# Kernel tuning notes

Hardware: AMD Instinct MI355X
Metric: run time of the kernel (lower is better)

## Reference

```python
import jax, jax.numpy as jnp
import numpy as np

D_K = 128


def setup_inputs() -> dict:
    key = jax.random.key(0)
    ks = jax.random.split(key, 10)
    B, S, D, TP, TE, DK = 4, 4096, 1024, 16, 64, D_K
    sc = lambda fan_in: 1.0 / np.sqrt(fan_in)
    return {
        "x": jax.random.normal(ks[0], (B, S, D), jnp.float32),
        "time_points": jax.random.normal(ks[1], (B, TP, TE), jnp.float32),
        "Wq": jax.random.normal(ks[2], (D, DK), jnp.float32) * sc(D),
        "bq": jnp.zeros((DK,), jnp.float32),
        "Wk": jax.random.normal(ks[3], (D, DK), jnp.float32) * sc(D),
        "bk": jnp.zeros((DK,), jnp.float32),
        "Wv": jax.random.normal(ks[4], (D, DK), jnp.float32) * sc(D),
        "bv": jnp.zeros((DK,), jnp.float32),
        "Wt": jax.random.normal(ks[5], (TE, DK), jnp.float32) * sc(TE),
        "bt": jnp.zeros((DK,), jnp.float32),
    }


def reference(x, time_points, Wq, bq, Wk, bk, Wv, bv, Wt, bt):
    B, S, _ = x.shape
    Q = x @ Wq + bq              # [B,S,dk]
    K = x @ Wk + bk              # [B,S,dk]
    V = x @ Wv + bv              # [B,S,dk]
    E = time_points @ Wt + bt    # [B,TP,dk] = time_emb
    # T = repeat(E, S times along dim 1). Then T^T @ T = S * E^T E and
    # ||T||_F = sqrt(S) * ||E||_F, so we never materialize T.
    S_f = jnp.asarray(S, jnp.float32)
    EtE = jnp.einsum('btd,bte->bde', E, E)            # [B,dk,dk]
    T_norm = jnp.sqrt(S_f * jnp.sum(E * E, axis=(1, 2), keepdims=False))  # [B]
    T_scaled = (S_f * EtE) / (T_norm[:, None, None] + 1e-8)  # [B,dk,dk]
    QT = jnp.einsum('bsd,bde->bse', Q, T_scaled)      # [B,S,dk]
    scores = jnp.einsum('bse,bte->bst', QT, K)        # [B,S,S]
    scores = scores / jnp.sqrt(jnp.asarray(D_K, jnp.float32))
    attn = jax.nn.softmax(scores, axis=-1)            # [B,S,S]
    out = jnp.einsum('bst,btd->bsd', attn, V)         # [B,S,dk]
    return out, attn
```

## Files before the change

### kernel.cpp

```cpp
#include <hip/hip_runtime.h>
#include <math.h>

#define BB 4
#define SS 4096
#define DD 1024
#define TPp 16
#define TEe 64
#define DKk 128

typedef __attribute__((ext_vector_type(8))) short short8;
typedef __attribute__((ext_vector_type(4))) float floatx4;
typedef __attribute__((ext_vector_type(16))) float floatx16;

#define BSTRIDE 524288
#define WFRAG 131072

static __device__ inline short f2bf(float f) {
  union { float f; unsigned u; } v; v.f = f;
  unsigned r = v.u + 0x7fff + ((v.u >> 16) & 1);
  return (short)(r >> 16);
}
static __device__ inline float bf2f(short s) {
  union { unsigned u; float f; } v; v.u = ((unsigned)(unsigned short)s) << 16;
  return v.f;
}

__global__ __launch_bounds__(256) void temb_kernel(const float* __restrict__ tp,
                                                   const float* __restrict__ Wt,
                                                   const float* __restrict__ bt,
                                                   const float* __restrict__ bq,
                                                   float* __restrict__ Tws,
                                                   float* __restrict__ bqtws) {
  __shared__ float sE[TPp * DKk];
  __shared__ float sB[TPp];
  __shared__ float red[256];
  const int p = blockIdx.x, b = blockIdx.y;
  const int tid = threadIdx.x;
  float lsq = 0.f;
  for (int l = 0; l < 8; ++l) {
    int idx = tid + 256 * l;
    int i = idx >> 7, j = idx & 127;
    float a = bt[j];
    for (int c = 0; c < TEe; ++c)
      a += tp[((size_t)b * TPp + i) * TEe + c] * Wt[c * DKk + j];
    sE[idx] = a;
    lsq += a * a;
  }
  red[tid] = lsq;
  __syncthreads();
  for (int s2 = 128; s2 > 0; s2 >>= 1) {
    if (tid < s2) red[tid] += red[tid + s2];
    __syncthreads();
  }
  const float total = red[0];
  const float scale = (float)SS / (sqrtf((float)SS * total) + 1e-8f);
  if (tid < TPp) {
    float a = 0.f;
    for (int d2 = 0; d2 < DKk; ++d2) a += bq[d2] * sE[tid * DKk + d2];
    sB[tid] = a;
  }
  __syncthreads();
  for (int l = 0; l < 8; ++l) {
    int idx = p * 2048 + tid + 256 * l;
    int d2 = idx >> 7, e = idx & 127;
    float a = 0.f;
    #pragma unroll
    for (int t = 0; t < TPp; ++t) a += sE[t * DKk + d2] * sE[t * DKk + e];
    Tws[(size_t)b * DKk * DKk + idx] = scale * a;
  }
  if (p == 0 && tid < DKk) {
    float a = 0.f;
    #pragma unroll
    for (int t = 0; t < TPp; ++t) a += sB[t] * sE[t * DKk + tid];
    bqtws[b * DKk + tid] = scale * a;
  }
}

__global__ __launch_bounds__(128) void wqp_kernel(const float* __restrict__ Wq,
                                                  const float* __restrict__ Tws,
                                                  short* __restrict__ WqphF,
                                                  short* __restrict__ WqplF) {
  __shared__ float sW[DKk];
  const int m = blockIdx.x, b = blockIdx.y;
  const int e = threadIdx.x;
  sW[e] = Wq[(size_t)m * DKk + e];
  __syncthreads();
  const float* Tb = Tws + (size_t)b * DKk * DKk;
  float a = 0.f;
  #pragma unroll 8
  for (int d2 = 0; d2 < DKk; ++d2) a += sW[d2] * Tb[d2 * DKk + e];
  const size_t off = (size_t)b * WFRAG +
      (size_t)((e >> 5) * 64 + (m >> 4)) * 512 + (32 * ((m >> 3) & 1) + (e & 31)) * 8 +
      (m & 7);
  short hh = f2bf(a);
  WqphF[off] = hh;
  WqplF[off] = f2bf(a - bf2f(hh));
}

__global__ __launch_bounds__(256) void wcast_kernel(const float* __restrict__ Wk,
                                                    const float* __restrict__ Wv,
                                                    short* __restrict__ WkhF,
                                                    short* __restrict__ WklF,
                                                    short* __restrict__ WvhF,
                                                    short* __restrict__ WvlF) {
  const float* W = blockIdx.y ? Wv : Wk;
  short* H = blockIdx.y ? WvhF : WkhF;
  short* L = blockIdx.y ? WvlF : WklF;
  const int ks = blockIdx.x;
  const int wave = threadIdx.x >> 6, lane = threadIdx.x & 63;
  const int n = wave * 32 + (lane & 31);
  const int k0 = ks * 16 + (lane >> 5) * 8;
  short8 h, l;
  #pragma unroll
  for (int j = 0; j < 8; ++j) {
    float v = W[(size_t)(k0 + j) * DKk + n];
    short hh = f2bf(v);
    h[j] = hh;
    l[j] = f2bf(v - bf2f(hh));
  }
  const size_t off = ((size_t)wave * 64 + ks) * 512 + lane * 8;
  *(short8*)&H[off] = h;
  *(short8*)&L[off] = l;
}

__global__ __launch_bounds__(256, 2) void proj_kernel(const float* __restrict__ x,
                                                      const short* __restrict__ WqphF,
                                                      const short* __restrict__ WqplF,
                                                      const short* __restrict__ WkhF,
                                                      const short* __restrict__ WklF,
                                                      const short* __restrict__ WvhF,
                                                      const short* __restrict__ WvlF,
                                                      const float* __restrict__ bqt,
                                                      const float* __restrict__ bk,
                                                      const float* __restrict__ bv,
                                                      short* __restrict__ QTh,
                                                      short* __restrict__ QTl,
                                                      short* __restrict__ Kh,
                                                      short* __restrict__ Kl,
                                                      short* __restrict__ VT) {
  __shared__ float xs[32 * 66];
  const int tileG = blockIdx.x;
  const int b = tileG >> 7, tileL = tileG & 127;
  const int rowbase = tileG * 32;
  const int tid = threadIdx.x, wave = tid >> 6, lane = tid & 63;
  const int l31 = lane & 31, half = lane >> 5;
  const short* B0h = WqphF + (size_t)b * WFRAG + (size_t)wave * 32768;
  const short* B0l = WqplF + (size_t)b * WFRAG + (size_t)wave * 32768;
  const short* B1h = WkhF + (size_t)wave * 32768;
  const short* B1l = WklF + (size_t)wave * 32768;
  const short* B2h = WvhF + (size_t)wave * 32768;
  const short* B2l = WvlF + (size_t)wave * 32768;
  floatx16 acc0, acc1, acc2;
  #pragma unroll
  for (int r = 0; r < 16; ++r) { acc0[r] = 0.f; acc1[r] = 0.f; acc2[r] = 0.f; }
  const int sr = tid >> 3, sc = (tid & 7) * 8;
  const float* xrow = &x[(size_t)(rowbase + sr) * DD + sc];
  float4 p0 = *(const float4*)xrow;
  float4 p1 = *(const float4*)(xrow + 4);
  for (int kc = 0; kc < 16; ++kc) {
    __syncthreads();
    float* dst = &xs[sr * 66 + sc];
    dst[0] = p0.x; dst[1] = p0.y; dst[2] = p0.z; dst[3] = p0.w;
    dst[4] = p1.x; dst[5] = p1.y; dst[6] = p1.z; dst[7] = p1.w;
    if (kc < 15) {
      p0 = *(const float4*)(xrow + (kc + 1) * 64);
      p1 = *(const float4*)(xrow + (kc + 1) * 64 + 4);
    }
    __syncthreads();
    #pragma unroll
    for (int ks = 0; ks < 4; ++ks) {
      const float* ap = &xs[l31 * 66 + ks * 16 + half * 8];
      short8 aH, aL;
      #pragma unroll
      for (int j = 0; j < 8; ++j) {
        float v = ap[j];
        short hh = f2bf(v);
        aH[j] = hh;
        aL[j] = f2bf(v - bf2f(hh));
      }
      const size_t boff = (size_t)(kc * 4 + ks) * 512 + lane * 8;
      short8 bh, bl;
      bh = *(const short8*)(B0h + boff); bl = *(const short8*)(B0l + boff);
      acc0 = __builtin_amdgcn_mfma_f32_32x32x16_bf16(aL, bh, acc0, 0, 0, 0);
      acc0 = __builtin_amdgcn_mfma_f32_32x32x16_bf16(aH, bl, acc0, 0, 0, 0);
      acc0 = __builtin_amdgcn_mfma_f32_32x32x16_bf16(aH, bh, acc0, 0, 0, 0);
      bh = *(const short8*)(B1h + boff); bl = *(const short8*)(B1l + boff);
      acc1 = __builtin_amdgcn_mfma_f32_32x32x16_bf16(aL, bh, acc1, 0, 0, 0);
      acc1 = __builtin_amdgcn_mfma_f32_32x32x16_bf16(aH, bl, acc1, 0, 0, 0);
      acc1 = __builtin_amdgcn_mfma_f32_32x32x16_bf16(aH, bh, acc1, 0, 0, 0);
      bh = *(const short8*)(B2h + boff); bl = *(const short8*)(B2l + boff);
      acc2 = __builtin_amdgcn_mfma_f32_32x32x16_bf16(aL, bh, acc2, 0, 0, 0);
      acc2 = __builtin_amdgcn_mfma_f32_32x32x16_bf16(aH, bl, acc2, 0, 0, 0);
      acc2 = __builtin_amdgcn_mfma_f32_32x32x16_bf16(aH, bh, acc2, 0, 0, 0);
    }
  }
  const int f = wave * 32 + l31;
  const int fks = f >> 4, fh = (f >> 3) & 1, fj = f & 7;
  const size_t qkbase =
      (size_t)b * BSTRIDE + (size_t)tileL * 4096 + (size_t)fks * 512 + fj;
  const float biasq = bqt[b * DKk + f];
  const float biask = bk[f];
  #pragma unroll
  for (int reg = 0; reg < 16; ++reg) {
    const int t = (reg & 3) + 8 * (reg >> 2) + 4 * half;
    const size_t off = qkbase + (size_t)(fh * 32 + t) * 8;
    float v = acc0[reg] + biasq;
    short hh = f2bf(v);
    QTh[off] = hh;
    QTl[off] = f2bf(v - bf2f(hh));
    v = acc1[reg] + biask;
    hh = f2bf(v);
    Kh[off] = hh;
    Kl[off] = f2bf(v - bf2f(hh));
  }
  const float biasv = bv[f];
  const int n15 = f & 15, ntt = f >> 4;
  #pragma unroll
  for (int g = 0; g < 4; ++g) {
    short4 s4;
    s4.x = f2bf(acc2[4 * g + 0] + biasv);
    s4.y = f2bf(acc2[4 * g + 1] + biasv);
    s4.z = f2bf(acc2[4 * g + 2] + biasv);
    s4.w = f2bf(acc2[4 * g + 3] + biasv);
    const size_t off = (size_t)b * BSTRIDE + (size_t)(tileL * 8 + ntt) * 512 +
                       (size_t)(g * 16 + n15) * 8 + 4 * half;
    *(short4*)&VT[off] = s4;
  }
}

__global__ __launch_bounds__(256, 2) void score_kernel(const short* __restrict__ QTh,
                                                       const short* __restrict__ QTl,
                                                       const short* __restrict__ Kh,
                                                       const short* __restrict__ Kl,
                                                       float* __restrict__ attn,
                                                       float* __restrict__ mrow,
                                                       float* __restrict__ linv) {
  __shared__ float smM[4][32], smL[4][32];
  const int id = blockIdx.x;
  const int xcd = id & 7;
  const int b = xcd >> 1;
  const int tile = ((id >> 3) << 1) + (xcd & 1);
  const int rowbase = tile * 32;
  const int tid = threadIdx.x;
  const int wave = tid >> 6, lane = tid & 63;
  const int l31 = lane & 31, half = lane >> 5;
  const float sc = 0.088388347648318447f;
  const size_t qbase = (size_t)b * BSTRIDE + (size_t)tile * 4096 + lane * 8;
  short8 aH[8], aL[8];
  #pragma unroll
  for (int ks = 0; ks < 8; ++ks) {
    aH[ks] = *(const short8*)(QTh + qbase + ks * 512);
    aL[ks] = *(const short8*)(QTl + qbase + ks * 512);
  }
  float m_r[16], l_r[16];
  #pragma unroll
  for (int r = 0; r < 16; ++r) { m_r[r] = -INFINITY; l_r[r] = 0.f; }
  float* attnb = attn + (size_t)b * SS * SS;
  float* srowbase = attnb + (size_t)rowbase * SS + l31;
  for (int ct = wave; ct < 128; ct += 4) {
    const int colbase = ct * 32;
    const size_t kbase = (size_t)b * BSTRIDE + (size_t)ct * 4096 + lane * 8;
    floatx16 acc;
    #pragma unroll
    for (int r = 0; r < 16; ++r) acc[r] = 0.f;
    #pragma unroll
    for (int ks = 0; ks < 8; ++ks) {
      short8 bh = *(const short8*)(Kh + kbase + ks * 512);
      short8 bl = *(const short8*)(Kl + kbase + ks * 512);
      acc = __builtin_amdgcn_mfma_f32_32x32x16_bf16(aH[ks], bh, acc, 0, 0, 0);
      acc = __builtin_amdgcn_mfma_f32_32x32x16_bf16(aH[ks], bl, acc, 0, 0, 0);
      acc = __builtin_amdgcn_mfma_f32_32x32x16_bf16(aL[ks], bh, acc, 0, 0, 0);
    }
    float* srow = srowbase + colbase;
    #pragma unroll
    for (int reg = 0; reg < 16; ++reg) {
      const int row = (reg & 3) + 8 * (reg >> 2) + 4 * half;
      const float s = acc[reg] * sc;
      __builtin_nontemporal_store(s, &srow[(size_t)row * SS]);
      const float mn = fmaxf(m_r[reg], s);
      l_r[reg] = l_r[reg] * __expf(m_r[reg] - mn) + __expf(s - mn);
      m_r[reg] = mn;
    }
  }
  #pragma unroll
  for (int off = 1; off < 32; off <<= 1) {
    #pragma unroll
    for (int reg = 0; reg < 16; ++reg) {
      const float mo = __shfl_xor(m_r[reg], off, 64);
      const float lo = __shfl_xor(l_r[reg], off, 64);
      const float mn = fmaxf(m_r[reg], mo);
      l_r[reg] = l_r[reg] * __expf(m_r[reg] - mn) + lo * __expf(mo - mn);
      m_r[reg] = mn;
    }
  }
  if (l31 == 0) {
    #pragma unroll
    for (int reg = 0; reg < 16; ++reg) {
      const int row = (reg & 3) + 8 * (reg >> 2) + 4 * half;
      smM[wave][row] = m_r[reg];
      smL[wave][row] = l_r[reg];
    }
  }
  __syncthreads();
  if (tid < 32) {
    float m = smM[0][tid], l = smL[0][tid];
    #pragma unroll
    for (int w = 1; w < 4; ++w) {
      const float mo = smM[w][tid], lo = smL[w][tid];
      const float mn = fmaxf(m, mo);
      l = l * __expf(m - mn) + lo * __expf(mo - mn);
      m = mn;
    }
    mrow[b * SS + rowbase + tid] = m;
    linv[b * SS + rowbase + tid] = 1.0f / l;
  }
}

__global__ __launch_bounds__(512, 4) void pv_kernel(const short* __restrict__ VT,
                                                    float* __restrict__ attn,
                                                    const float* __restrict__ mrow,
                                                    const float* __restrict__ linv,
                                                    float* __restrict__ outp) {
  __shared__ float sAcc[3][2][16][128];
  const int id = blockIdx.x;
  const int xcd = id & 7;
  const int b = xcd >> 1;
  const int tile = ((id >> 3) << 1) + (xcd & 1);
  const int rowbase = tile * 32;
  const int tid = threadIdx.x, wave = tid >> 6, lane = tid & 63;
  const int wg = wave & 1, th = wave >> 1;
  const int l15 = lane & 15, quad = lane >> 4;
  const int row = rowbase + wg * 16 + l15;
  const float m_i = mrow[b * SS + row];
  const float li = linv[b * SS + row];
  float* arow = attn + (size_t)b * SS * SS + (size_t)row * SS + quad * 8;
  const short* vtb = VT + (size_t)b * BSTRIDE + lane * 8;
  floatx4 acc[8];
  #pragma unroll
  for (int nt = 0; nt < 8; ++nt)
    #pragma unroll
    for (int r = 0; r < 4; ++r) acc[nt][r] = 0.f;
  for (int ct = th; ct < 128; ct += 4) {
    const int t0 = ct * 32;
    floatx4 s0 = __builtin_nontemporal_load((const floatx4*)(arow + t0));
    floatx4 s1 = __builtin_nontemporal_load((const floatx4*)(arow + t0 + 4));
    float p[8];
    p[0] = __expf(s0.x - m_i) * li; p[1] = __expf(s0.y - m_i) * li;
    p[2] = __expf(s0.z - m_i) * li; p[3] = __expf(s0.w - m_i) * li;
    p[4] = __expf(s1.x - m_i) * li; p[5] = __expf(s1.y - m_i) * li;
    p[6] = __expf(s1.z - m_i) * li; p[7] = __expf(s1.w - m_i) * li;
    floatx4 o0 = {p[0], p[1], p[2], p[3]};
    floatx4 o1 = {p[4], p[5], p[6], p[7]};
    __builtin_nontemporal_store(o0, (floatx4*)(arow + t0));
    __builtin_nontemporal_store(o1, (floatx4*)(arow + t0 + 4));
    short8 a;
    #pragma unroll
    for (int j = 0; j < 8; ++j) a[j] = f2bf(p[j]);
    const short* vtc = vtb + (size_t)ct * 4096;
    #pragma unroll
    for (int nt = 0; nt < 8; ++nt) {
      short8 bf = *(const short8*)(vtc + nt * 512);
      acc[nt] = __builtin_amdgcn_mfma_f32_16x16x32_bf16(a, bf, acc[nt], 0, 0, 0);
    }
  }
  if (th > 0) {
    #pragma unroll
    for (int nt = 0; nt < 8; ++nt)
      #pragma unroll
      for (int r = 0; r < 4; ++r)
        sAcc[th - 1][wg][quad * 4 + r][nt * 16 + l15] = acc[nt][r];
  }
  __syncthreads();
  if (th == 0) {
    #pragma unroll
    for (int nt = 0; nt < 8; ++nt)
      #pragma unroll
      for (int r = 0; r < 4; ++r) {
        const int rr = quad * 4 + r, cc = nt * 16 + l15;
        outp[((size_t)b * SS + rowbase + wg * 16 + rr) * DKk + cc] =
            acc[nt][r] + sAcc[0][wg][rr][cc] + sAcc[1][wg][rr][cc] + sAcc[2][wg][rr][cc];
      }
  }
}

extern "C" void kernel_launch(void* const* d_in, const int* in_sizes, int n_in,
                              void* d_out, int out_size, void* d_ws, size_t ws_size,
                              hipStream_t stream) {
  const float* x  = (const float*)d_in[0];
  const float* tp = (const float*)d_in[1];
  const float* Wq = (const float*)d_in[2];
  const float* bq = (const float*)d_in[3];
  const float* Wk = (const float*)d_in[4];
  const float* bk = (const float*)d_in[5];
  const float* Wv = (const float*)d_in[6];
  const float* bv = (const float*)d_in[7];
  const float* Wt = (const float*)d_in[8];
  const float* bt = (const float*)d_in[9];
  float* out  = (float*)d_out;
  float* attn = out + (size_t)BB * SS * DKk;
  float* ws = (float*)d_ws;
  float* Tws   = ws;
  float* bqt   = ws + 65536;
  short* WqphF = (short*)(ws + 66048);
  short* WqplF = (short*)(ws + 328192);
  short* WkhF  = (short*)(ws + 590336);
  short* WklF  = (short*)(ws + 655872);
  short* WvhF  = (short*)(ws + 721408);
  short* WvlF  = (short*)(ws + 786944);
  short* QTh   = (short*)(ws + 852480);
  short* QTl   = (short*)(ws + 1901056);
  short* Kh    = (short*)(ws + 2949632);
  short* Kl    = (short*)(ws + 3998208);
  short* VT    = (short*)(ws + 5046784);
  float* mrow  = ws + 6095360;
  float* lin   = ws + 6111744;

  temb_kernel<<<dim3(8, 4), 256, 0, stream>>>(tp, Wt, bt, bq, Tws, bqt);
  wqp_kernel<<<dim3(1024, 4), 128, 0, stream>>>(Wq, Tws, WqphF, WqplF);
  wcast_kernel<<<dim3(64, 2), 256, 0, stream>>>(Wk, Wv, WkhF, WklF, WvhF, WvlF);
  proj_kernel<<<512, 256, 0, stream>>>(x, WqphF, WqplF, WkhF, WklF, WvhF, WvlF,
                                       bqt, bk, bv, QTh, QTl, Kh, Kl, VT);
  score_kernel<<<512, 256, 0, stream>>>(QTh, QTl, Kh, Kl, attn, mrow, lin);
  pv_kernel<<<512, 512, 0, stream>>>(VT, attn, mrow, lin, out);
}
```

Baseline: 699.7 us.

## Recompute scores in PV pass instead of writing and rereading attention matrix

Splits the work into an ml_kernel that computes QK^T only to get the row max and sum (without storing scores) and a pv_kernel that recomputes QK^T, writes the normalized probabilities once and multiplies by V. This removes one full fp32 S×S write plus read of the attention matrix (256MB each) in exchange for doing the 3-MFMA split-bf16 score GEMM twice. The V layout is changed so the PV product can use 32x32 MFMAs fed directly from transposed score fragments via cross-half shuffles.

```diff
diff --git a/kernel.cpp b/kernel.cpp
--- a/kernel.cpp
+++ b/kernel.cpp
@@ -214,7 +214,6 @@
     Kl[off] = f2bf(v - bf2f(hh));
   }
   const float biasv = bv[f];
-  const int n15 = f & 15, ntt = f >> 4;
   #pragma unroll
   for (int g = 0; g < 4; ++g) {
     short4 s4;
@@ -222,20 +221,94 @@
     s4.y = f2bf(acc2[4 * g + 1] + biasv);
     s4.z = f2bf(acc2[4 * g + 2] + biasv);
     s4.w = f2bf(acc2[4 * g + 3] + biasv);
-    const size_t off = (size_t)b * BSTRIDE + (size_t)(tileL * 8 + ntt) * 512 +
-                       (size_t)(g * 16 + n15) * 8 + 4 * half;
+    const size_t off = (size_t)b * BSTRIDE +
+        (size_t)(wave * 256 + tileL * 2 + (g >> 1)) * 512 +
+        (size_t)((g & 1) * 32 + l31) * 8 + 4 * half;
     *(short4*)&VT[off] = s4;
   }
 }
 
-__global__ __launch_bounds__(256, 2) void score_kernel(const short* __restrict__ QTh,
-                                                       const short* __restrict__ QTl,
-                                                       const short* __restrict__ Kh,
-                                                       const short* __restrict__ Kl,
-                                                       float* __restrict__ attn,
-                                                       float* __restrict__ mrow,
-                                                       float* __restrict__ linv) {
+__global__ __launch_bounds__(256, 2) void ml_kernel(const short* __restrict__ QTh,
+                                                    const short* __restrict__ QTl,
+                                                    const short* __restrict__ Kh,
+                                                    const short* __restrict__ Kl,
+                                                    float* __restrict__ mrow,
+                                                    float* __restrict__ linv) {
   __shared__ float smM[4][32], smL[4][32];
+  const int id = blockIdx.x;
+  const int xcd = id & 7;
+  const int b = xcd >> 1;
+  const int tile = ((id >> 3) << 1) + (xcd & 1);
+  const int rowbase = tile * 32;
+  const int tid = threadIdx.x;
+  const int wave = tid >> 6, lane = tid & 63;
+  const int l31 = lane & 31;
+  const float sc = 0.088388347648318447f;
+  const size_t qbase = (size_t)b * BSTRIDE + (size_t)tile * 4096 + lane * 8;
+  short8 qh[8], ql[8];
+  #pragma unroll
+  for (int ks = 0; ks < 8; ++ks) {
+    qh[ks] = *(const short8*)(QTh + qbase + ks * 512);
+    ql[ks] = *(const short8*)(QTl + qbase + ks * 512);
+  }
+  float m = -INFINITY, l = 0.f;
+  for (int ct = wave; ct < 128; ct += 4) {
+    const size_t kbase = (size_t)b * BSTRIDE + (size_t)ct * 4096 + lane * 8;
+    floatx16 acc;
+    #pragma unroll
+    for (int r = 0; r < 16; ++r) acc[r] = 0.f;
+    #pragma unroll
+    for (int ks = 0; ks < 8; ++ks) {
+      short8 kh = *(const short8*)(Kh + kbase + ks * 512);
+      short8 kl = *(const short8*)(Kl + kbase + ks * 512);
+      acc = __builtin_amdgcn_mfma_f32_32x32x16_bf16(kh, qh[ks], acc, 0, 0, 0);
+      acc = __builtin_amdgcn_mfma_f32_32x32x16_bf16(kh, ql[ks], acc, 0, 0, 0);
+      acc = __builtin_amdgcn_mfma_f32_32x32x16_bf16(kl, qh[ks], acc, 0, 0, 0);
+    }
+    float s[16];
+    float tmax = -INFINITY;
+    #pragma unroll
+    for (int r = 0; r < 16; ++r) { s[r] = acc[r] * sc; tmax = fmaxf(tmax, s[r]); }
+    const float mn = fmaxf(m, tmax);
+    float ps = 0.f;
+    #pragma unroll
+    for (int r = 0; r < 16; ++r) ps += __expf(s[r] - mn);
+    l = l * __expf(m - mn) + ps;
+    m = mn;
+  }
+  {
+    const float mo = __shfl_xor(m, 32, 64);
+    const float lo = __shfl_xor(l, 32, 64);
+    const float mn = fmaxf(m, mo);
+    l = l * __expf(m - mn) + lo * __expf(mo - mn);
+    m = mn;
+  }
+  if (lane < 32) { smM[wave][l31] = m; smL[wave][l31] = l; }
+  __syncthreads();
+  if (tid < 32) {
+    float mm = smM[0][tid], ll = smL[0][tid];
+    #pragma unroll
+    for (int w = 1; w < 4; ++w) {
+      const float mo = smM[w][tid], lo = smL[w][tid];
+      const float mn = fmaxf(mm, mo);
+      ll = ll * __expf(mm - mn) + lo * __expf(mo - mn);
+      mm = mn;
+    }
+    mrow[b * SS + rowbase + tid] = mm;
+    linv[b * SS + rowbase + tid] = 1.0f / ll;
+  }
+}
+
+__global__ __launch_bounds__(256, 2) void pv_kernel(const short* __restrict__ QTh,
+                                                    const short* __restrict__ QTl,
+                                                    const short* __restrict__ Kh,
+                                                    const short* __restrict__ Kl,
+                                                    const short* __restrict__ VT,
+                                                    float* __restrict__ attn,
+                                                    const float* __restrict__ mrow,
+                                                    const float* __restrict__ linv,
+                                                    float* __restrict__ outp) {
+  __shared__ float sAcc[3][4][64][16];
   const int id = blockIdx.x;
   const int xcd = id & 7;
   const int b = xcd >> 1;
@@ -246,139 +319,78 @@
   const int l31 = lane & 31, half = lane >> 5;
   const float sc = 0.088388347648318447f;
   const size_t qbase = (size_t)b * BSTRIDE + (size_t)tile * 4096 + lane * 8;
-  short8 aH[8], aL[8];
+  short8 qh[8], ql[8];
   #pragma unroll
   for (int ks = 0; ks < 8; ++ks) {
-    aH[ks] = *(const short8*)(QTh + qbase + ks * 512);
-    aL[ks] = *(const short8*)(QTl + qbase + ks * 512);
-  }
-  float m_r[16], l_r[16];
-  #pragma unroll
-  for (int r = 0; r < 16; ++r) { m_r[r] = -INFINITY; l_r[r] = 0.f; }
-  float* attnb = attn + (size_t)b * SS * SS;
-  float* srowbase = attnb + (size_t)rowbase * SS + l31;
+    qh[ks] = *(const short8*)(QTh + qbase + ks * 512);
+    ql[ks] = *(const short8*)(QTl + qbase + ks * 512);
+  }
+  const float m_i = mrow[b * SS + rowbase + l31];
+  const float li = linv[b * SS + rowbase + l31];
+  float* arow = attn + (size_t)b * SS * SS + (size_t)(rowbase + l31) * SS + 4 * half;
+  const short* vtb = VT + (size_t)b * BSTRIDE + lane * 8;
+  floatx16 pacc[4];
+  #pragma unroll
+  for (int dt = 0; dt < 4; ++dt)
+    #pragma unroll
+    for (int r = 0; r < 16; ++r) pacc[dt][r] = 0.f;
   for (int ct = wave; ct < 128; ct += 4) {
-    const int colbase = ct * 32;
     const size_t kbase = (size_t)b * BSTRIDE + (size_t)ct * 4096 + lane * 8;
     floatx16 acc;
     #pragma unroll
     for (int r = 0; r < 16; ++r) acc[r] = 0.f;
     #pragma unroll
     for (int ks = 0; ks < 8; ++ks) {
-      short8 bh = *(const short8*)(Kh + kbase + ks * 512);
-      short8 bl = *(const short8*)(Kl + kbase + ks * 512);
-      acc = __builtin_amdgcn_mfma_f32_32x32x16_bf16(aH[ks], bh, acc, 0, 0, 0);
-      acc = __builtin_amdgcn_mfma_f32_32x32x16_bf16(aH[ks], bl, acc, 0, 0, 0);
-      acc = __builtin_amdgcn_mfma_f32_32x32x16_bf16(aL[ks], bh, acc, 0, 0, 0);
-    }
-    float* srow = srowbase + colbase;
-    #pragma unroll
-    for (int reg = 0; reg < 16; ++reg) {
-      const int row = (reg & 3) + 8 * (reg >> 2) + 4 * half;
-      const float s = acc[reg] * sc;
-      __builtin_nontemporal_store(s, &srow[(size_t)row * SS]);
-      const float mn = fmaxf(m_r[reg], s);
-      l_r[reg] = l_r[reg] * __expf(m_r[reg] - mn) + __expf(s - mn);
-      m_r[reg] = mn;
-    }
-  }
-  #pragma unroll
-  for (int off = 1; off < 32; off <<= 1) {
-    #pragma unroll
-    for (int reg = 0; reg < 16; ++reg) {
-      const float mo = __shfl_xor(m_r[reg], off, 64);
-      const float lo = __shfl_xor(l_r[reg], off, 64);
-      const float mn = fmaxf(m_r[reg], mo);
-      l_r[reg] = l_r[reg] * __expf(m_r[reg] - mn) + lo * __expf(mo - mn);
-      m_r[reg] = mn;
-    }
-  }
-  if (l31 == 0) {
-    #pragma unroll
-    for (int reg = 0; reg < 16; ++reg) {
-      const int row = (reg & 3) + 8 * (reg >> 2) + 4 * half;
-      smM[wave][row] = m_r[reg];
-      smL[wave][row] = l_r[reg];
-    }
+      short8 kh = *(const short8*)(Kh + kbase + ks * 512);
+      short8 kl = *(const short8*)(Kl + kbase + ks * 512);
+      acc = __builtin_amdgcn_mfma_f32_32x32x16_bf16(kh, qh[ks], acc, 0, 0, 0);
+      acc = __builtin_amdgcn_mfma_f32_32x32x16_bf16(kh, ql[ks], acc, 0, 0, 0);
+      acc = __builtin_amdgcn_mfma_f32_32x32x16_bf16(kl, qh[ks], acc, 0, 0, 0);
+    }
+    float p[16];
+    #pragma unroll
+    for (int r = 0; r < 16; ++r) p[r] = __expf(acc[r] * sc - m_i) * li;
+    #pragma unroll
+    for (int g = 0; g < 4; ++g) {
+      floatx4 o = {p[4 * g], p[4 * g + 1], p[4 * g + 2], p[4 * g + 3]};
+      __builtin_nontemporal_store(o, (floatx4*)(arow + ct * 32 + 8 * g));
+    }
+    short8 af0, af1;
+    #pragma unroll
+    for (int rr = 0; rr < 4; ++rr) {
+      const float shl = __shfl_xor(p[rr], 32, 64);
+      const float shh = __shfl_xor(p[rr + 4], 32, 64);
+      af0[rr] = f2bf(half ? shh : p[rr]);
+      af0[rr + 4] = f2bf(half ? p[rr + 4] : shl);
+      const float shl2 = __shfl_xor(p[rr + 8], 32, 64);
+      const float shh2 = __shfl_xor(p[rr + 12], 32, 64);
+      af1[rr] = f2bf(half ? shh2 : p[rr + 8]);
+      af1[rr + 4] = f2bf(half ? p[rr + 12] : shl2);
+    }
+    #pragma unroll
+    for (int dt = 0; dt < 4; ++dt) {
+      short8 v0 = *(const short8*)(vtb + (size_t)(dt * 256 + ct * 2) * 512);
+      pacc[dt] = __builtin_amdgcn_mfma_f32_32x32x16_bf16(af0, v0, pacc[dt], 0, 0, 0);
+      short8 v1 = *(const short8*)(vtb + (size_t)(dt * 256 + ct * 2 + 1) * 512);
+      pacc[dt] = __builtin_amdgcn_mfma_f32_32x32x16_bf16(af1, v1, pacc[dt], 0, 0, 0);
+    }
+  }
+  if (wave > 0) {
+    #pragma unroll
+    for (int dt = 0; dt < 4; ++dt)
+      #pragma unroll
+      for (int r = 0; r < 16; ++r) sAcc[wave - 1][dt][lane][r] = pacc[dt][r];
   }
   __syncthreads();
-  if (tid < 32) {
-    float m = smM[0][tid], l = smL[0][tid];
-    #pragma unroll
-    for (int w = 1; w < 4; ++w) {
-      const float mo = smM[w][tid], lo = smL[w][tid];
-      const float mn = fmaxf(m, mo);
-      l = l * __expf(m - mn) + lo * __expf(mo - mn);
-      m = mn;
-    }
-    mrow[b * SS + rowbase + tid] = m;
-    linv[b * SS + rowbase + tid] = 1.0f / l;
-  }
-}
-
-__global__ __launch_bounds__(512, 4) void pv_kernel(const short* __restrict__ VT,
-                                                    float* __restrict__ attn,
-                                                    const float* __restrict__ mrow,
-                                                    const float* __restrict__ linv,
-                                                    float* __restrict__ outp) {
-  __shared__ float sAcc[3][2][16][128];
-  const int id = blockIdx.x;
-  const int xcd = id & 7;
-  const int b = xcd >> 1;
-  const int tile = ((id >> 3) << 1) + (xcd & 1);
-  const int rowbase = tile * 32;
-  const int tid = threadIdx.x, wave = tid >> 6, lane = tid & 63;
-  const int wg = wave & 1, th = wave >> 1;
-  const int l15 = lane & 15, quad = lane >> 4;
-  const int row = rowbase + wg * 16 + l15;
-  const float m_i = mrow[b * SS + row];
-  const float li = linv[b * SS + row];
-  float* arow = attn + (size_t)b * SS * SS + (size_t)row * SS + quad * 8;
-  const short* vtb = VT + (size_t)b * BSTRIDE + lane * 8;
-  floatx4 acc[8];
-  #pragma unroll
-  for (int nt = 0; nt < 8; ++nt)
-    #pragma unroll
-    for (int r = 0; r < 4; ++r) acc[nt][r] = 0.f;
-  for (int ct = th; ct < 128; ct += 4) {
-    const int t0 = ct * 32;
-    floatx4 s0 = __builtin_nontemporal_load((const floatx4*)(arow + t0));
-    floatx4 s1 = __builtin_nontemporal_load((const floatx4*)(arow + t0 + 4));
-    float p[8];
-    p[0] = __expf(s0.x - m_i) * li; p[1] = __expf(s0.y - m_i) * li;
-    p[2] = __expf(s0.z - m_i) * li; p[3] = __expf(s0.w - m_i) * li;
-    p[4] = __expf(s1.x - m_i) * li; p[5] = __expf(s1.y - m_i) * li;
-    p[6] = __expf(s1.z - m_i) * li; p[7] = __expf(s1.w - m_i) * li;
-    floatx4 o0 = {p[0], p[1], p[2], p[3]};
-    floatx4 o1 = {p[4], p[5], p[6], p[7]};
-    __builtin_nontemporal_store(o0, (floatx4*)(arow + t0));
-    __builtin_nontemporal_store(o1, (floatx4*)(arow + t0 + 4));
-    short8 a;
-    #pragma unroll
-    for (int j = 0; j < 8; ++j) a[j] = f2bf(p[j]);
-    const short* vtc = vtb + (size_t)ct * 4096;
-    #pragma unroll
-    for (int nt = 0; nt < 8; ++nt) {
-      short8 bf = *(const short8*)(vtc + nt * 512);
-      acc[nt] = __builtin_amdgcn_mfma_f32_16x16x32_bf16(a, bf, acc[nt], 0, 0, 0);
-    }
-  }
-  if (th > 0) {
-    #pragma unroll
-    for (int nt = 0; nt < 8; ++nt)
+  if (wave == 0) {
+    #pragma unroll
+    for (int dt = 0; dt < 4; ++dt)
       #pragma unroll
-      for (int r = 0; r < 4; ++r)
-        sAcc[th - 1][wg][quad * 4 + r][nt * 16 + l15] = acc[nt][r];
-  }
-  __syncthreads();
-  if (th == 0) {
-    #pragma unroll
-    for (int nt = 0; nt < 8; ++nt)
-      #pragma unroll
-      for (int r = 0; r < 4; ++r) {
-        const int rr = quad * 4 + r, cc = nt * 16 + l15;
-        outp[((size_t)b * SS + rowbase + wg * 16 + rr) * DKk + cc] =
-            acc[nt][r] + sAcc[0][wg][rr][cc] + sAcc[1][wg][rr][cc] + sAcc[2][wg][rr][cc];
+      for (int r = 0; r < 16; ++r) {
+        const int q = (r & 3) + 8 * (r >> 2) + 4 * half;
+        const float v = pacc[dt][r] + sAcc[0][dt][lane][r] + sAcc[1][dt][lane][r] +
+                        sAcc[2][dt][lane][r];
+        outp[((size_t)b * SS + rowbase + q) * DKk + dt * 32 + l31] = v;
       }
   }
 }
@@ -420,6 +432,6 @@
   wcast_kernel<<<dim3(64, 2), 256, 0, stream>>>(Wk, Wv, WkhF, WklF, WvhF, WvlF);
   proj_kernel<<<512, 256, 0, stream>>>(x, WqphF, WqplF, WkhF, WklF, WvhF, WvlF,
                                        bqt, bk, bv, QTh, QTl, Kh, Kl, VT);
-  score_kernel<<<512, 256, 0, stream>>>(QTh, QTl, Kh, Kl, attn, mrow, lin);
-  pv_kernel<<<512, 512, 0, stream>>>(VT, attn, mrow, lin, out);
-}
+  ml_kernel<<<512, 256, 0, stream>>>(QTh, QTl, Kh, Kl, mrow, lin);
+  pv_kernel<<<512, 256, 0, stream>>>(QTh, QTl, Kh, Kl, VT, attn, mrow, lin, out);
+}
```

New measurement: 709.4 us. Within noise of the previous version (+1.4%).
